# Kernel optimization log

Hardware: AMD Instinct MI355X
Metric: run time of the kernel (lower is better)

## Reference

```python
import jax, jax.numpy as jnp
import numpy as np

B, T, ENC, DEC, A = 64, 2048, 1024, 1024, 512


def setup_inputs() -> dict:
    key = jax.random.key(0)
    k1, k2, k3, k4, k5 = jax.random.split(key, 5)
    return {
        "h_j": jax.random.normal(k1, (B, T, ENC), dtype=jnp.float32),
        "s_t": jax.random.normal(k2, (B, DEC), dtype=jnp.float32),
        "U_w": jax.random.normal(k3, (ENC, A), dtype=jnp.float32) * (ENC ** -0.5),
        "W_w": jax.random.normal(k4, (DEC, A), dtype=jnp.float32) * (DEC ** -0.5),
        "V_w": jax.random.normal(k5, (A, 1), dtype=jnp.float32) * (A ** -0.5),
    }


def reference(h_j, s_t, U_w, W_w, V_w):
    # f1: [B, T, A] ; f2: [B, 1, A]
    f1 = jnp.einsum("bte,ea->bta", h_j, U_w)
    f2 = (s_t @ W_w)[:, None, :]
    # additive score e_t: [B, T, 1]
    e_t = jnp.tanh(f1 + f2) @ V_w
    a_t = jax.nn.softmax(e_t, axis=1)            # softmax over sequence axis
    c_t = jnp.sum(a_t * h_j, axis=1, keepdims=True)  # [B, 1, ENC]
    return (c_t, a_t)
```

## Files before the change

kernel.cpp:

```cpp
#include <hip/hip_runtime.h>
#include <hip/hip_bf16.h>
#include <stdint.h>

#define B_   64
#define T_   2048
#define ENC_ 1024
#define DEC_ 1024
#define A_   512
#define M_   (B_ * T_)

#define BK   64
#define CH   64
#define NCH  (M_ / CH)
#define CPB  (T_ / CH)

typedef __bf16 bf16x8 __attribute__((ext_vector_type(8)));
typedef float  f32x4  __attribute__((ext_vector_type(4)));
typedef unsigned short u16;
typedef u16 u16x8 __attribute__((ext_vector_type(8)));

__device__ __forceinline__ float fast_tanh(float x) {
    float ax = fabsf(x);
    float e  = __expf(-2.0f * ax);
    float t  = (1.0f - e) / (1.0f + e);
    return copysignf(t, x);
}

__global__ __launch_bounds__(256) void k_transpose_U(
        const float* __restrict__ U, u16* __restrict__ Ut) {
    int idx = blockIdx.x * 256 + threadIdx.x;
    if (idx >= ENC_ * A_) return;
    int k = idx / A_, n = idx % A_;
    __bf16 v = (__bf16)U[idx];
    Ut[n * ENC_ + k] = *(u16*)&v;
}

__global__ __launch_bounds__(256) void k_f2(
        const float* __restrict__ s, const float* __restrict__ W,
        float* __restrict__ f2) {
    int b = blockIdx.x;
    int a0 = threadIdx.x;
    const float* srow = s + (size_t)b * DEC_;
    float acc0 = 0.f, acc1 = 0.f;
    for (int e = 0; e < DEC_; ++e) {
        float sv = srow[e];
        acc0 = fmaf(sv, W[(size_t)e * A_ + a0],       acc0);
        acc1 = fmaf(sv, W[(size_t)e * A_ + a0 + 256], acc1);
    }
    f2[(size_t)b * A_ + a0]       = acc0;
    f2[(size_t)b * A_ + a0 + 256] = acc1;
}

__global__ __launch_bounds__(512, 4) void k_gemm_fused(
        const float* __restrict__ h, const u16* __restrict__ Ut,
        const float* __restrict__ f2, const float* __restrict__ V,
        float* __restrict__ e_full, float* __restrict__ mpart,
        float* __restrict__ spart, float* __restrict__ opart) {
    __shared__ u16 Alds[2][CH * BK];
    __shared__ u16 Blds[A_ * BK];
    float* ered = (float*)&Alds[0][0];
    float* wlds = ered + 512;

    const int tid  = threadIdx.x;
    const int lane = tid & 63;
    const int wid  = tid >> 6;
    const int lr   = lane & 15;
    const int g    = lane >> 4;
    const int sw   = (lr & 7) << 3;

    const int d      = blockIdx.x;
    const int gchunk = (d & 7) * 256 + (d >> 3);
    const int brow   = gchunk * CH;
    const int b      = gchunk >> 5;
    const int chunk  = gchunk & 31;

    f32x4 acc[4][4] = {};
    f32x4 ar[2];

    const int arow = tid >> 3;
    const int acol = (tid & 7) * 8;
    auto loadA = [&](int kt) {
        const float* srcA = h + (size_t)(brow + arow) * ENC_ + kt * BK + acol;
        ar[0] = *(const f32x4*)srcA;
        ar[1] = *(const f32x4*)(srcA + 4);
    };
    auto writeA = [&](int buf) {
        u16x8 w;
#pragma unroll
        for (int j = 0; j < 4; ++j) {
            __bf16 lo = (__bf16)ar[0][j], hi = (__bf16)ar[1][j];
            w[j]     = *(u16*)&lo;
            w[j + 4] = *(u16*)&hi;
        }
        *(u16x8*)&Alds[buf][(tid * 8) ^ ((arow & 7) << 3)] = w;
    };
    auto stageB = [&](int kt) {
#pragma unroll
        for (int it = 0; it < 8; ++it) {
            int G  = it * 512 + tid;
            int n  = G >> 3;
            int kc = ((G & 7) ^ (n & 7)) << 3;
            const u16* src = Ut + (size_t)n * ENC_ + kt * BK + kc;
            u16* dst = &Blds[(size_t)(it * 512 + wid * 64) * 8];
            __builtin_amdgcn_global_load_lds(
                (const __attribute__((address_space(1))) void*)src,
                (__attribute__((address_space(3))) void*)dst, 16, 0, 0);
        }
    };
    auto compute = [&](int cur) {
#pragma unroll
        for (int kk = 0; kk < 2; ++kk) {
            bf16x8 af[4], bfr[4];
#pragma unroll
            for (int mf = 0; mf < 4; ++mf)
                af[mf] = *(const bf16x8*)&Alds[cur][
                    (((mf * 16 + lr) * 64) + kk * 32 + g * 8) ^ sw];
#pragma unroll
            for (int nf = 0; nf < 4; ++nf)
                bfr[nf] = *(const bf16x8*)&Blds[
                    (((wid * 64 + nf * 16 + lr) * 64) + kk * 32 + g * 8) ^ sw];
#pragma unroll
            for (int mf = 0; mf < 4; ++mf)
#pragma unroll
                for (int nf = 0; nf < 4; ++nf)
                    acc[mf][nf] = __builtin_amdgcn_mfma_f32_16x16x32_bf16(
                        af[mf], bfr[nf], acc[mf][nf], 0, 0, 0);
        }
    };

    loadA(0);
    writeA(0);
    stageB(0);
    __syncthreads();

    for (int kt = 0; kt < ENC_ / BK; ++kt) {
        const int cur = kt & 1;
        if (kt + 1 < ENC_ / BK) loadA(kt + 1);
        compute(cur);
        if (kt + 1 < ENC_ / BK) {
            writeA(cur ^ 1);
            __syncthreads();
            stageB(kt + 1);
            __syncthreads();
        }
    }

    float vv[4], ff[4];
#pragma unroll
    for (int nf = 0; nf < 4; ++nf) {
        int n = wid * 64 + nf * 16 + lr;
        vv[nf] = V[n];
        ff[nf] = f2[(size_t)b * A_ + n];
    }
#pragma unroll
    for (int mf = 0; mf < 4; ++mf) {
        float sums[4];
#pragma unroll
        for (int i = 0; i < 4; ++i) {
            float sv = 0.f;
#pragma unroll
            for (int nf = 0; nf < 4; ++nf) {
                float x = acc[mf][nf][i] + ff[nf];
                sv = fmaf(fast_tanh(x), vv[nf], sv);
            }
#pragma unroll
            for (int mm = 1; mm < 16; mm <<= 1)
                sv += __shfl_xor(sv, mm, 64);
            sums[i] = sv;
        }
        if (lr == 0) {
#pragma unroll
            for (int i = 0; i < 4; ++i)
                ered[wid * 64 + mf * 16 + g * 4 + i] = sums[i];
        }
    }
    __syncthreads();

    if (tid < 64) {
        float er = 0.f;
#pragma unroll
        for (int w = 0; w < 8; ++w) er += ered[w * 64 + tid];
        float mb = er;
#pragma unroll
        for (int mm = 1; mm < 64; mm <<= 1)
            mb = fmaxf(mb, __shfl_xor(mb, mm, 64));
        float wr_ = __expf(er - mb);
        float sb = wr_;
#pragma unroll
        for (int mm = 1; mm < 64; mm <<= 1)
            sb += __shfl_xor(sb, mm, 64);
        wlds[tid] = wr_;
        e_full[(size_t)b * T_ + chunk * CH + tid] = er;
        if (tid == 0) { mpart[gchunk] = mb; spart[gchunk] = sb; }
    }
    __syncthreads();

    const int c2 = tid * 2;
    float o0 = 0.f, o1 = 0.f;
#pragma unroll 8
    for (int r = 0; r < CH; ++r) {
        float w = wlds[r];
        float2 hv = *(const float2*)(h + (size_t)(brow + r) * ENC_ + c2);
        o0 = fmaf(w, hv.x, o0);
        o1 = fmaf(w, hv.y, o1);
    }
    float* op = opart + (size_t)gchunk * ENC_ + c2;
    op[0] = o0; op[1] = o1;
}

__global__ __launch_bounds__(256) void k_ctx_reduce(
        const float* __restrict__ mpart, const float* __restrict__ spart,
        const float* __restrict__ opart, float* __restrict__ c_out,
        float* __restrict__ mg_g, float* __restrict__ sg_g) {
    const int b = blockIdx.x, tid = threadIdx.x;
    __shared__ float esc[CPB];
    __shared__ float mgS, sgS;

    if (tid < CPB) {
        float mr = mpart[b * CPB + tid];
        float sr = spart[b * CPB + tid];
        float mg = mr;
#pragma unroll
        for (int mm = 1; mm < 32; mm <<= 1)
            mg = fmaxf(mg, __shfl_xor(mg, mm, 32));
        float e = __expf(mr - mg);
        esc[tid] = e;
        float S = sr * e;
#pragma unroll
        for (int mm = 1; mm < 32; mm <<= 1)
            S += __shfl_xor(S, mm, 32);
        if (tid == 0) { mgS = mg; sgS = S; mg_g[b] = mg; sg_g[b] = S; }
    }
    __syncthreads();
    float inv = 1.0f / sgS;
    int c = tid * 4;
    f32x4 av = {0.f, 0.f, 0.f, 0.f};
    for (int r = 0; r < CPB; ++r) {
        f32x4 ov = *(const f32x4*)&opart[((size_t)(b * CPB + r)) * ENC_ + c];
        float e = esc[r];
        av[0] = fmaf(e, ov[0], av[0]); av[1] = fmaf(e, ov[1], av[1]);
        av[2] = fmaf(e, ov[2], av[2]); av[3] = fmaf(e, ov[3], av[3]);
    }
    av[0] *= inv; av[1] *= inv; av[2] *= inv; av[3] *= inv;
    *(f32x4*)&c_out[(size_t)b * ENC_ + c] = av;
}

__global__ __launch_bounds__(256) void k_a_final(
        const float* __restrict__ e_full, const float* __restrict__ mg_g,
        const float* __restrict__ sg_g, float* __restrict__ a_out) {
    int idx = blockIdx.x * 256 + threadIdx.x;
    int b = idx >> 11;
    a_out[idx] = __expf(e_full[idx] - mg_g[b]) / sg_g[b];
}

__global__ __launch_bounds__(512, 4) void k_gemm_e_fb(
        const float* __restrict__ h, const u16* __restrict__ Ut,
        const float* __restrict__ f2, const float* __restrict__ V,
        float* __restrict__ e_part) {
    __shared__ u16 Alds[128 * BK];
    __shared__ u16 Blds[256 * BK];
    const int tid = threadIdx.x, lane = tid & 63, wid = tid >> 6;
    const int wr = wid >> 2, wc = wid & 3, lr = lane & 15, g = lane >> 4;
    const int sw = (lr & 7) << 3;
    const int d = blockIdx.x, xcd = d & 7, s = d >> 3, m = s & 1;
    const int pair = xcd * 128 + (s >> 1);
    const int brow = pair * 128, bcol = m * 256, b = brow / T_;
    f32x4 acc[4][4] = {};
    for (int kt = 0; kt < ENC_ / BK; ++kt) {
        const int k0 = kt * BK;
#pragma unroll
        for (int it = 0; it < 4; ++it) {
            int G = it * 512 + tid, n = G >> 3;
            int kc = ((G & 7) ^ (n & 7)) << 3;
            const u16* src = Ut + (size_t)(bcol + n) * ENC_ + k0 + kc;
            u16* dst = &Blds[(size_t)(it * 512 + wid * 64) * 8];
            __builtin_amdgcn_global_load_lds(
                (const __attribute__((address_space(1))) void*)src,
                (__attribute__((address_space(3))) void*)dst, 16, 0, 0);
        }
#pragma unroll
        for (int it = 0; it < 2; ++it) {
            int flat = (it * 512 + tid) * 8, r = flat >> 6, c = flat & 63;
            const float* srcA = h + (size_t)(brow + r) * ENC_ + k0 + c;
            f32x4 v0 = *(const f32x4*)srcA, v1 = *(const f32x4*)(srcA + 4);
            u16x8 w;
#pragma unroll
            for (int j = 0; j < 4; ++j) {
                __bf16 lo = (__bf16)v0[j], hi = (__bf16)v1[j];
                w[j] = *(u16*)&lo; w[j + 4] = *(u16*)&hi;
            }
            *(u16x8*)&Alds[flat ^ ((r & 7) << 3)] = w;
        }
        __syncthreads();
#pragma unroll
        for (int kk = 0; kk < 2; ++kk) {
            bf16x8 af[4], bfr[4];
#pragma unroll
            for (int mf = 0; mf < 4; ++mf)
                af[mf] = *(const bf16x8*)&Alds[(((wr * 64 + mf * 16 + lr) * 64) + kk * 32 + g * 8) ^ sw];
#pragma unroll
            for (int nf = 0; nf < 4; ++nf)
                bfr[nf] = *(const bf16x8*)&Blds[(((wc * 64 + nf * 16 + lr) * 64) + kk * 32 + g * 8) ^ sw];
#pragma unroll
            for (int mf = 0; mf < 4; ++mf)
#pragma unroll
                for (int nf = 0; nf < 4; ++nf)
                    acc[mf][nf] = __builtin_amdgcn_mfma_f32_16x16x32_bf16(
                        af[mf], bfr[nf], acc[mf][nf], 0, 0, 0);
        }
        __syncthreads();
    }
    float vv[4], ff[4];
#pragma unroll
    for (int nf = 0; nf < 4; ++nf) {
        int n = bcol + wc * 64 + nf * 16 + lr;
        vv[nf] = V[n]; ff[nf] = f2[(size_t)b * A_ + n];
    }
    const int p = m * 4 + wc;
    float* ep = e_part + (size_t)p * M_ + brow + wr * 64;
#pragma unroll
    for (int mf = 0; mf < 4; ++mf) {
        float sums[4];
#pragma unroll
        for (int i = 0; i < 4; ++i) {
            float sv = 0.f;
#pragma unroll
            for (int nf = 0; nf < 4; ++nf)
                sv = fmaf(fast_tanh(acc[mf][nf][i] + ff[nf]), vv[nf], sv);
#pragma unroll
            for (int mm = 1; mm < 16; mm <<= 1) sv += __shfl_xor(sv, mm, 64);
            sums[i] = sv;
        }
        if (lr == 0)
#pragma unroll
            for (int i = 0; i < 4; ++i) ep[mf * 16 + g * 4 + i] = sums[i];
    }
}

__global__ __launch_bounds__(256) void k_softmax_fb(
        const float* __restrict__ e_part, float* __restrict__ a_out) {
    const int b = blockIdx.x, tid = threadIdx.x;
    const int lane = tid & 63, w = tid >> 6;
    __shared__ float red[4], red2[4];
    float ls[8]; float lmax = -1e30f;
#pragma unroll
    for (int i = 0; i < 8; ++i) {
        size_t mm = (size_t)b * T_ + i * 256 + tid;
        float sv = 0.f;
#pragma unroll
        for (int p = 0; p < 8; ++p) sv += e_part[(size_t)p * M_ + mm];
        ls[i] = sv; lmax = fmaxf(lmax, sv);
    }
#pragma unroll
    for (int mm = 1; mm < 64; mm <<= 1) lmax = fmaxf(lmax, __shfl_xor(lmax, mm, 64));
    if (lane == 0) red[w] = lmax;
    __syncthreads();
    float bmax = fmaxf(fmaxf(red[0], red[1]), fmaxf(red[2], red[3]));
    float lsum = 0.f;
#pragma unroll
    for (int i = 0; i < 8; ++i) { ls[i] = __expf(ls[i] - bmax); lsum += ls[i]; }
#pragma unroll
    for (int mm = 1; mm < 64; mm <<= 1) lsum += __shfl_xor(lsum, mm, 64);
    if (lane == 0) red2[w] = lsum;
    __syncthreads();
    float inv = 1.0f / (red2[0] + red2[1] + red2[2] + red2[3]);
#pragma unroll
    for (int i = 0; i < 8; ++i)
        a_out[(size_t)b * T_ + i * 256 + tid] = ls[i] * inv;
}

__global__ __launch_bounds__(256) void k_ctx_part_fb(
        const float* __restrict__ h, const float* __restrict__ a,
        float* __restrict__ c_part) {
    const int b = blockIdx.x, tc = blockIdx.y, tid = threadIdx.x;
    __shared__ float alds[128];
    if (tid < 128) alds[tid] = a[(size_t)b * T_ + tc * 128 + tid];
    __syncthreads();
    float4 acc = {0.f, 0.f, 0.f, 0.f};
    const float* hb = h + ((size_t)b * T_ + (size_t)tc * 128) * ENC_ + tid * 4;
    for (int t = 0; t < 128; ++t) {
        float av = alds[t];
        float4 hv = *(const float4*)(hb + (size_t)t * ENC_);
        acc.x = fmaf(av, hv.x, acc.x); acc.y = fmaf(av, hv.y, acc.y);
        acc.z = fmaf(av, hv.z, acc.z); acc.w = fmaf(av, hv.w, acc.w);
    }
    *(float4*)&c_part[((size_t)(tc * 64 + b)) * ENC_ + tid * 4] = acc;
}

__global__ __launch_bounds__(256) void k_ctx_final_fb(
        const float* __restrict__ c_part, float* __restrict__ c_out) {
    int idx = blockIdx.x * 256 + threadIdx.x;
    int off = idx * 4;
    float4 sv = {0.f, 0.f, 0.f, 0.f};
#pragma unroll
    for (int tc = 0; tc < 16; ++tc) {
        float4 v = *(const float4*)&c_part[(size_t)tc * 64 * 1024 + off];
        sv.x += v.x; sv.y += v.y; sv.z += v.z; sv.w += v.w;
    }
    *(float4*)&c_out[off] = sv;
}

extern "C" void kernel_launch(void* const* d_in, const int* in_sizes, int n_in,
                              void* d_out, int out_size, void* d_ws, size_t ws_size,
                              hipStream_t stream) {
    const float* h = (const float*)d_in[0];
    const float* s = (const float*)d_in[1];
    const float* U = (const float*)d_in[2];
    const float* W = (const float*)d_in[3];
    const float* V = (const float*)d_in[4];

    float* out   = (float*)d_out;
    float* c_out = out;
    float* a_out = out + 64 * 1024;

    char* ws = (char*)d_ws;
    u16*   Ut = (u16*)ws;
    float* f2 = (float*)(ws + (1 << 20));

    k_transpose_U<<<2048, 256, 0, stream>>>(U, Ut);
    k_f2<<<64, 256, 0, stream>>>(s, W, f2);

    const size_t NEED = (size_t)10 * 1024 * 1024 + (64 << 10);
    if (ws_size >= NEED) {
        float* e_full = (float*)(ws + 0x120000);
        float* mpart  = (float*)(ws + 0x1A0000);
        float* spart  = (float*)(ws + 0x1A2000);
        float* mg_g   = (float*)(ws + 0x1A4000);
        float* sg_g   = (float*)(ws + 0x1A4100);
        float* opart  = (float*)(ws + 0x200000);

        k_gemm_fused<<<NCH, 512, 0, stream>>>(h, Ut, f2, V,
                                              e_full, mpart, spart, opart);
        k_ctx_reduce<<<64, 256, 0, stream>>>(mpart, spart, opart,
                                             c_out, mg_g, sg_g);
        k_a_final<<<M_ / 256, 256, 0, stream>>>(e_full, mg_g, sg_g, a_out);
    } else {
        float* e_part = (float*)(ws + (1 << 20) + (128 << 10));
        float* c_part = e_part;
        k_gemm_e_fb<<<2048, 512, 0, stream>>>(h, Ut, f2, V, e_part);
        k_softmax_fb<<<64, 256, 0, stream>>>(e_part, a_out);
        dim3 gc(64, 16);
        k_ctx_part_fb<<<gc, 256, 0, stream>>>(h, a_out, c_part);
        k_ctx_final_fb<<<64, 256, 0, stream>>>(c_part, c_out);
    }
}
```

Measured before the change: 313.0 us.

## Pipeline fused GEMM main loop with manual waitcnt barriers and tiled U transpose

Restructures the fused GEMM k-loop to replace the two __syncthreads per tile with explicit vmcnt/lgkmcnt waits and a single raw barrier. The next B tile's LDS staging is issued between the two MFMA halves so global loads overlap compute. B staging is remapped so each wave fills its own contiguous LDS slice, and the U transpose now goes through a shared-memory tile so both its reads and writes are coalesced. The fallback path for small workspaces is removed; the manual waitcnt ordering risks races if the count assumptions are wrong.

```diff
diff --git a/kernel.cpp b/kernel.cpp
--- a/kernel.cpp
+++ b/kernel.cpp
@@ -13,6 +13,7 @@
 #define CH   64
 #define NCH  (M_ / CH)
 #define CPB  (T_ / CH)
+#define NT   (ENC_ / BK)
 
 typedef __bf16 bf16x8 __attribute__((ext_vector_type(8)));
 typedef float  f32x4  __attribute__((ext_vector_type(4)));
@@ -28,11 +29,23 @@
 
 __global__ __launch_bounds__(256) void k_transpose_U(
         const float* __restrict__ U, u16* __restrict__ Ut) {
-    int idx = blockIdx.x * 256 + threadIdx.x;
-    if (idx >= ENC_ * A_) return;
-    int k = idx / A_, n = idx % A_;
-    __bf16 v = (__bf16)U[idx];
-    Ut[n * ENC_ + k] = *(u16*)&v;
+    __shared__ float tl[64][65];
+    const int k0 = blockIdx.x * 64;
+    const int n0 = blockIdx.y * 64;
+    const int tr = threadIdx.x >> 6;
+    const int tc = threadIdx.x & 63;
+#pragma unroll
+    for (int i = 0; i < 16; ++i) {
+        int r = i * 4 + tr;
+        tl[r][tc] = U[(size_t)(k0 + r) * A_ + n0 + tc];
+    }
+    __syncthreads();
+#pragma unroll
+    for (int i = 0; i < 16; ++i) {
+        int nn = i * 4 + tr;
+        __bf16 v = (__bf16)tl[tc][nn];
+        Ut[(size_t)(n0 + nn) * ENC_ + k0 + tc] = *(u16*)&v;
+    }
 }
 
 __global__ __launch_bounds__(256) void k_f2(
@@ -94,54 +107,67 @@
         }
         *(u16x8*)&Alds[buf][(tid * 8) ^ ((arow & 7) << 3)] = w;
     };
+    u16* const bslice = &Blds[(size_t)wid * 64 * 64];
     auto stageB = [&](int kt) {
 #pragma unroll
         for (int it = 0; it < 8; ++it) {
-            int G  = it * 512 + tid;
-            int n  = G >> 3;
-            int kc = ((G & 7) ^ (n & 7)) << 3;
+            int n  = wid * 64 + it * 8 + (lane >> 3);
+            int kc = ((lane & 7) ^ (n & 7)) << 3;
             const u16* src = Ut + (size_t)n * ENC_ + kt * BK + kc;
-            u16* dst = &Blds[(size_t)(it * 512 + wid * 64) * 8];
+            u16* dst = bslice + (size_t)it * 512;
             __builtin_amdgcn_global_load_lds(
                 (const __attribute__((address_space(1))) void*)src,
                 (__attribute__((address_space(3))) void*)dst, 16, 0, 0);
         }
     };
-    auto compute = [&](int cur) {
-#pragma unroll
-        for (int kk = 0; kk < 2; ++kk) {
-            bf16x8 af[4], bfr[4];
-#pragma unroll
-            for (int mf = 0; mf < 4; ++mf)
-                af[mf] = *(const bf16x8*)&Alds[cur][
-                    (((mf * 16 + lr) * 64) + kk * 32 + g * 8) ^ sw];
+    auto readAB = [&](int cur, int kk, bf16x8 (&af)[4], bf16x8 (&bfr)[4]) {
+#pragma unroll
+        for (int mf = 0; mf < 4; ++mf)
+            af[mf] = *(const bf16x8*)&Alds[cur][
+                (((mf * 16 + lr) * 64) + kk * 32 + g * 8) ^ sw];
+#pragma unroll
+        for (int nf = 0; nf < 4; ++nf)
+            bfr[nf] = *(const bf16x8*)&Blds[
+                (((wid * 64 + nf * 16 + lr) * 64) + kk * 32 + g * 8) ^ sw];
+    };
+    auto mfma16 = [&](bf16x8 (&af)[4], bf16x8 (&bfr)[4]) {
+#pragma unroll
+        for (int mf = 0; mf < 4; ++mf)
 #pragma unroll
             for (int nf = 0; nf < 4; ++nf)
-                bfr[nf] = *(const bf16x8*)&Blds[
-                    (((wid * 64 + nf * 16 + lr) * 64) + kk * 32 + g * 8) ^ sw];
-#pragma unroll
-            for (int mf = 0; mf < 4; ++mf)
-#pragma unroll
-                for (int nf = 0; nf < 4; ++nf)
-                    acc[mf][nf] = __builtin_amdgcn_mfma_f32_16x16x32_bf16(
-                        af[mf], bfr[nf], acc[mf][nf], 0, 0, 0);
-        }
-    };
+                acc[mf][nf] = __builtin_amdgcn_mfma_f32_16x16x32_bf16(
+                    af[mf], bfr[nf], acc[mf][nf], 0, 0, 0);
+    };
+
+#define RBAR()  __builtin_amdgcn_s_barrier()
+#define LGKM0() asm volatile("s_waitcnt lgkmcnt(0)" ::: "memory")
+#define VMC(n)  asm volatile("s_waitcnt vmcnt(" #n ")" ::: "memory")
 
     loadA(0);
+    stageB(0);
     writeA(0);
-    stageB(0);
-    __syncthreads();
-
-    for (int kt = 0; kt < ENC_ / BK; ++kt) {
+    LGKM0();
+    RBAR();
+
+    for (int kt = 0; kt < NT; ++kt) {
         const int cur = kt & 1;
-        if (kt + 1 < ENC_ / BK) loadA(kt + 1);
-        compute(cur);
-        if (kt + 1 < ENC_ / BK) {
+        if (kt + 1 < NT) {
+            loadA(kt + 1);
+            VMC(2);
+        } else {
+            VMC(0);
+        }
+        bf16x8 af[4], bfr[4];
+        readAB(cur, 0, af, bfr);
+        mfma16(af, bfr);
+        readAB(cur, 1, af, bfr);
+        LGKM0();
+        if (kt + 1 < NT) stageB(kt + 1);
+        mfma16(af, bfr);
+        if (kt + 1 < NT) {
             writeA(cur ^ 1);
-            __syncthreads();
-            stageB(kt + 1);
-            __syncthreads();
+            LGKM0();
+            RBAR();
         }
     }
 
@@ -206,6 +232,9 @@
     }
     float* op = opart + (size_t)gchunk * ENC_ + c2;
     op[0] = o0; op[1] = o1;
+#undef RBAR
+#undef LGKM0
+#undef VMC
 }
 
 __global__ __launch_bounds__(256) void k_ctx_reduce(
@@ -253,153 +282,6 @@
     a_out[idx] = __expf(e_full[idx] - mg_g[b]) / sg_g[b];
 }
 
-__global__ __launch_bounds__(512, 4) void k_gemm_e_fb(
-        const float* __restrict__ h, const u16* __restrict__ Ut,
-        const float* __restrict__ f2, const float* __restrict__ V,
-        float* __restrict__ e_part) {
-    __shared__ u16 Alds[128 * BK];
-    __shared__ u16 Blds[256 * BK];
-    const int tid = threadIdx.x, lane = tid & 63, wid = tid >> 6;
-    const int wr = wid >> 2, wc = wid & 3, lr = lane & 15, g = lane >> 4;
-    const int sw = (lr & 7) << 3;
-    const int d = blockIdx.x, xcd = d & 7, s = d >> 3, m = s & 1;
-    const int pair = xcd * 128 + (s >> 1);
-    const int brow = pair * 128, bcol = m * 256, b = brow / T_;
-    f32x4 acc[4][4] = {};
-    for (int kt = 0; kt < ENC_ / BK; ++kt) {
-        const int k0 = kt * BK;
-#pragma unroll
-        for (int it = 0; it < 4; ++it) {
-            int G = it * 512 + tid, n = G >> 3;
-            int kc = ((G & 7) ^ (n & 7)) << 3;
-            const u16* src = Ut + (size_t)(bcol + n) * ENC_ + k0 + kc;
-            u16* dst = &Blds[(size_t)(it * 512 + wid * 64) * 8];
-            __builtin_amdgcn_global_load_lds(
-                (const __attribute__((address_space(1))) void*)src,
-                (__attribute__((address_space(3))) void*)dst, 16, 0, 0);
-        }
-#pragma unroll
-        for (int it = 0; it < 2; ++it) {
-            int flat = (it * 512 + tid) * 8, r = flat >> 6, c = flat & 63;
-            const float* srcA = h + (size_t)(brow + r) * ENC_ + k0 + c;
-            f32x4 v0 = *(const f32x4*)srcA, v1 = *(const f32x4*)(srcA + 4);
-            u16x8 w;
-#pragma unroll
-            for (int j = 0; j < 4; ++j) {
-                __bf16 lo = (__bf16)v0[j], hi = (__bf16)v1[j];
-                w[j] = *(u16*)&lo; w[j + 4] = *(u16*)&hi;
-            }
-            *(u16x8*)&Alds[flat ^ ((r & 7) << 3)] = w;
-        }
-        __syncthreads();
-#pragma unroll
-        for (int kk = 0; kk < 2; ++kk) {
-            bf16x8 af[4], bfr[4];
-#pragma unroll
-            for (int mf = 0; mf < 4; ++mf)
-                af[mf] = *(const bf16x8*)&Alds[(((wr * 64 + mf * 16 + lr) * 64) + kk * 32 + g * 8) ^ sw];
-#pragma unroll
-            for (int nf = 0; nf < 4; ++nf)
-                bfr[nf] = *(const bf16x8*)&Blds[(((wc * 64 + nf * 16 + lr) * 64) + kk * 32 + g * 8) ^ sw];
-#pragma unroll
-            for (int mf = 0; mf < 4; ++mf)
-#pragma unroll
-                for (int nf = 0; nf < 4; ++nf)
-                    acc[mf][nf] = __builtin_amdgcn_mfma_f32_16x16x32_bf16(
-                        af[mf], bfr[nf], acc[mf][nf], 0, 0, 0);
-        }
-        __syncthreads();
-    }
-    float vv[4], ff[4];
-#pragma unroll
-    for (int nf = 0; nf < 4; ++nf) {
-        int n = bcol + wc * 64 + nf * 16 + lr;
-        vv[nf] = V[n]; ff[nf] = f2[(size_t)b * A_ + n];
-    }
-    const int p = m * 4 + wc;
-    float* ep = e_part + (size_t)p * M_ + brow + wr * 64;
-#pragma unroll
-    for (int mf = 0; mf < 4; ++mf) {
-        float sums[4];
-#pragma unroll
-        for (int i = 0; i < 4; ++i) {
-            float sv = 0.f;
-#pragma unroll
-            for (int nf = 0; nf < 4; ++nf)
-                sv = fmaf(fast_tanh(acc[mf][nf][i] + ff[nf]), vv[nf], sv);
-#pragma unroll
-            for (int mm = 1; mm < 16; mm <<= 1) sv += __shfl_xor(sv, mm, 64);
-            sums[i] = sv;
-        }
-        if (lr == 0)
-#pragma unroll
-            for (int i = 0; i < 4; ++i) ep[mf * 16 + g * 4 + i] = sums[i];
-    }
-}
-
-__global__ __launch_bounds__(256) void k_softmax_fb(
-        const float* __restrict__ e_part, float* __restrict__ a_out) {
-    const int b = blockIdx.x, tid = threadIdx.x;
-    const int lane = tid & 63, w = tid >> 6;
-    __shared__ float red[4], red2[4];
-    float ls[8]; float lmax = -1e30f;
-#pragma unroll
-    for (int i = 0; i < 8; ++i) {
-        size_t mm = (size_t)b * T_ + i * 256 + tid;
-        float sv = 0.f;
-#pragma unroll
-        for (int p = 0; p < 8; ++p) sv += e_part[(size_t)p * M_ + mm];
-        ls[i] = sv; lmax = fmaxf(lmax, sv);
-    }
-#pragma unroll
-    for (int mm = 1; mm < 64; mm <<= 1) lmax = fmaxf(lmax, __shfl_xor(lmax, mm, 64));
-    if (lane == 0) red[w] = lmax;
-    __syncthreads();
-    float bmax = fmaxf(fmaxf(red[0], red[1]), fmaxf(red[2], red[3]));
-    float lsum = 0.f;
-#pragma unroll
-    for (int i = 0; i < 8; ++i) { ls[i] = __expf(ls[i] - bmax); lsum += ls[i]; }
-#pragma unroll
-    for (int mm = 1; mm < 64; mm <<= 1) lsum += __shfl_xor(lsum, mm, 64);
-    if (lane == 0) red2[w] = lsum;
-    __syncthreads();
-    float inv = 1.0f / (red2[0] + red2[1] + red2[2] + red2[3]);
-#pragma unroll
-    for (int i = 0; i < 8; ++i)
-        a_out[(size_t)b * T_ + i * 256 + tid] = ls[i] * inv;
-}
-
-__global__ __launch_bounds__(256) void k_ctx_part_fb(
-        const float* __restrict__ h, const float* __restrict__ a,
-        float* __restrict__ c_part) {
-    const int b = blockIdx.x, tc = blockIdx.y, tid = threadIdx.x;
-    __shared__ float alds[128];
-    if (tid < 128) alds[tid] = a[(size_t)b * T_ + tc * 128 + tid];
-    __syncthreads();
-    float4 acc = {0.f, 0.f, 0.f, 0.f};
-    const float* hb = h + ((size_t)b * T_ + (size_t)tc * 128) * ENC_ + tid * 4;
-    for (int t = 0; t < 128; ++t) {
-        float av = alds[t];
-        float4 hv = *(const float4*)(hb + (size_t)t * ENC_);
-        acc.x = fmaf(av, hv.x, acc.x); acc.y = fmaf(av, hv.y, acc.y);
-        acc.z = fmaf(av, hv.z, acc.z); acc.w = fmaf(av, hv.w, acc.w);
-    }
-    *(float4*)&c_part[((size_t)(tc * 64 + b)) * ENC_ + tid * 4] = acc;
-}
-
-__global__ __launch_bounds__(256) void k_ctx_final_fb(
-        const float* __restrict__ c_part, float* __restrict__ c_out) {
-    int idx = blockIdx.x * 256 + threadIdx.x;
-    int off = idx * 4;
-    float4 sv = {0.f, 0.f, 0.f, 0.f};
-#pragma unroll
-    for (int tc = 0; tc < 16; ++tc) {
-        float4 v = *(const float4*)&c_part[(size_t)tc * 64 * 1024 + off];
-        sv.x += v.x; sv.y += v.y; sv.z += v.z; sv.w += v.w;
-    }
-    *(float4*)&c_out[off] = sv;
-}
-
 extern "C" void kernel_launch(void* const* d_in, const int* in_sizes, int n_in,
                               void* d_out, int out_size, void* d_ws, size_t ws_size,
                               hipStream_t stream) {
@@ -416,31 +298,20 @@
     char* ws = (char*)d_ws;
     u16*   Ut = (u16*)ws;
     float* f2 = (float*)(ws + (1 << 20));
-
-    k_transpose_U<<<2048, 256, 0, stream>>>(U, Ut);
+    float* e_full = (float*)(ws + 0x120000);
+    float* mpart  = (float*)(ws + 0x1A0000);
+    float* spart  = (float*)(ws + 0x1A2000);
+    float* mg_g   = (float*)(ws + 0x1A4000);
+    float* sg_g   = (float*)(ws + 0x1A4100);
+    float* opart  = (float*)(ws + 0x200000);
+
+    dim3 gt(ENC_ / 64, A_ / 64);
+    k_transpose_U<<<gt, 256, 0, stream>>>(U, Ut);
     k_f2<<<64, 256, 0, stream>>>(s, W, f2);
 
-    const size_t NEED = (size_t)10 * 1024 * 1024 + (64 << 10);
-    if (ws_size >= NEED) {
-        float* e_full = (float*)(ws + 0x120000);
-        float* mpart  = (float*)(ws + 0x1A0000);
-        float* spart  = (float*)(ws + 0x1A2000);
-        float* mg_g   = (float*)(ws + 0x1A4000);
-        float* sg_g   = (float*)(ws + 0x1A4100);
-        float* opart  = (float*)(ws + 0x200000);
-
-        k_gemm_fused<<<NCH, 512, 0, stream>>>(h, Ut, f2, V,
-                                              e_full, mpart, spart, opart);
-        k_ctx_reduce<<<64, 256, 0, stream>>>(mpart, spart, opart,
-                                             c_out, mg_g, sg_g);
-        k_a_final<<<M_ / 256, 256, 0, stream>>>(e_full, mg_g, sg_g, a_out);
-    } else {
-        float* e_part = (float*)(ws + (1 << 20) + (128 << 10));
-        float* c_part = e_part;
-        k_gemm_e_fb<<<2048, 512, 0, stream>>>(h, Ut, f2, V, e_part);
-        k_softmax_fb<<<64, 256, 0, stream>>>(e_part, a_out);
-        dim3 gc(64, 16);
-        k_ctx_part_fb<<<gc, 256, 0, stream>>>(h, a_out, c_part);
-        k_ctx_final_fb<<<64, 256, 0, stream>>>(c_part, c_out);
-    }
-}
+    k_gemm_fused<<<NCH, 512, 0, stream>>>(h, Ut, f2, V,
+                                          e_full, mpart, spart, opart);
+    k_ctx_reduce<<<64, 256, 0, stream>>>(mpart, spart, opart,
+                                         c_out, mg_g, sg_g);
+    k_a_final<<<M_ / 256, 256, 0, stream>>>(e_full, mg_g, sg_g, a_out);
+}
```

Measured after the change: 322.0 us. +2.9%, slower.
